# Optimization experiments

Measured on AMD Instinct MI355X. Metric: run time of the kernel, lower is better.

## Reference

```python
import jax, jax.numpy as jnp
import numpy as np

B = 1024
D = 768          # 2 * hidden_size
HID = 384        # hidden_size (split point for mu/sigma)
MLP_H = 300      # InfoNCE hidden size
LOG2PI = float(np.log(2.0 * np.pi))


def setup_inputs() -> dict:
    key = jax.random.key(0)
    ks = jax.random.split(key, 12)
    s = 0.02
    return {
        "zl": jax.random.normal(ks[0], (B, 20, D), jnp.float32),
        "zv": jax.random.normal(ks[1], (B, 36, D), jnp.float32),
        "fc_l_w": jax.random.normal(ks[2], (20,), jnp.float32) * s,
        "fc_l_b": jax.random.normal(ks[3], (), jnp.float32) * s,
        "fc_v_w": jax.random.normal(ks[4], (36,), jnp.float32) * s,
        "fc_v_b": jax.random.normal(ks[5], (), jnp.float32) * s,
        "W1": jax.random.normal(ks[6], (MLP_H, 2 * HID), jnp.float32) * s,
        "b1": jnp.zeros((MLP_H,), jnp.float32),
        "W2": jax.random.normal(ks[7], (1, MLP_H), jnp.float32) * s,
        "b2": jnp.zeros((1,), jnp.float32),
        "eps1": jax.random.normal(ks[8], (B, HID), jnp.float32),
        "eps2": jax.random.normal(ks[9], (B, HID), jnp.float32),
        "perm": jax.random.permutation(ks[10], B),
    }


def _log_prob(mu, sigma, x):
    # Independent(Normal(mu, sigma), 1).log_prob(x)
    z = (x - mu) / sigma
    return jnp.sum(-jnp.log(sigma) - 0.5 * LOG2PI - 0.5 * z * z, axis=-1)


def reference(zl, zv, fc_l_w, fc_l_b, fc_v_w, fc_v_b, W1, b1, W2, b2, eps1, eps2, perm):
    # fc over token dim: permute(0,2,1) @ Linear(20->1) -> [B, D]
    z1 = jnp.einsum('bsd,s->bd', zl, fc_l_w) + fc_l_b
    z2 = jnp.einsum('bsd,s->bd', zv, fc_v_w) + fc_v_b

    mu1, sig1 = z1[:, :HID], jax.nn.softplus(z1[:, HID:]) + 1e-7
    mu2, sig2 = z2[:, :HID], jax.nn.softplus(z2[:, HID:]) + 1e-7

    # rsample
    s1 = mu1 + sig1 * eps1  # [B, HID]
    s2 = mu2 + sig2 * eps2

    kl_1_2 = _log_prob(mu1, sig1, s1) - _log_prob(mu2, sig2, s1)
    kl_2_1 = _log_prob(mu2, sig2, s2) - _log_prob(mu1, sig1, s2)
    d_skl = jnp.mean(kl_1_2 + kl_2_1) / 2.0

    # InfoNCE(x=s1, y=s2): F(x,y) = softplus(relu([x,y]W1^T + b1) W2^T + b2)
    W1x, W1y = W1[:, :HID], W1[:, HID:]
    Ax = s1 @ W1x.T            # [B, MLP_H], x contribution
    By = s2 @ W1y.T            # [B, MLP_H], y contribution
    w2 = W2[0]                 # [MLP_H]

    # T0: matched pairs
    T0 = jax.nn.softplus(jax.nn.relu(Ax + By + b1) @ w2 + b2[0])  # [B]

    # T1[i, j] = F(x_j, y_perm[i]); tile via broadcasting instead of repeat+cat
    By_p = By[perm]                                             # [B, MLP_H]
    h = jax.nn.relu(Ax[None, :, :] + By_p[:, None, :] + b1)     # [B, B, MLP_H]
    T1 = jax.nn.softplus(h @ w2 + b2[0])                        # [B, B]

    lower_bound = T0.mean() - (jax.scipy.special.logsumexp(T1, axis=1).mean() - jnp.log(jnp.float32(B)))
    return d_skl - lower_bound
```

## Files before the change

kernel.cpp:

```cpp
#include <hip/hip_runtime.h>
#include <math.h>

#define BB   1024
#define DD   768
#define HIDV 384
#define MLPH 300
#define MLPP 320

typedef float v2f __attribute__((ext_vector_type(2)));

__device__ __forceinline__ float softplusf(float x) {
    return (x > 20.f) ? x : log1pf(expf(x));
}

__device__ __forceinline__ void f4arr(float4 v, float* o) {
    o[0] = v.x; o[1] = v.y; o[2] = v.z; o[3] = v.w;
}

__global__ void k_init(float* __restrict__ ws) {
    int i = blockIdx.x * 256 + threadIdx.x;
    if (i < 16 + BB) ws[i] = 0.f;
}

__global__ __launch_bounds__(384, 6) void k_rs(
    const float* __restrict__ zl, const float* __restrict__ zv,
    const float* __restrict__ wl, const float* __restrict__ blp,
    const float* __restrict__ wv, const float* __restrict__ bvp,
    const float* __restrict__ eps1, const float* __restrict__ eps2,
    float* __restrict__ s1, float* __restrict__ s2, float* __restrict__ accum)
{
    int b = blockIdx.x;
    int t = threadIdx.x;
    int half = (t >= 192) ? 1 : 0;
    int col = t - half * 192;
    int ofl = half * 10;
    int ofv = half * 18;
    const float4* zl4 = (const float4*)zl + b * (20 * 192) + ofl * 192 + col;
    const float4* zv4 = (const float4*)zv + b * (36 * 192) + ofv * 192 + col;

    float z1v[4] = {0,0,0,0}, z2v[4] = {0,0,0,0};

    #pragma unroll
    for (int sp = 0; sp < 10; ++sp) {
        float w = wl[sp + ofl];
        float a[4];
        f4arr(zl4[sp * 192], a);
        #pragma unroll
        for (int j = 0; j < 4; ++j) z1v[j] = fmaf(a[j], w, z1v[j]);
    }
    #pragma unroll
    for (int sp = 0; sp < 18; ++sp) {
        float w = wv[sp + ofv];
        float a[4];
        f4arr(zv4[sp * 192], a);
        #pragma unroll
        for (int j = 0; j < 4; ++j) z2v[j] = fmaf(a[j], w, z2v[j]);
    }

    __shared__ __align__(16) float p1[192 * 4];
    __shared__ __align__(16) float p2[192 * 4];
    if (half) {
        ((float4*)p1)[col] = make_float4(z1v[0], z1v[1], z1v[2], z1v[3]);
        ((float4*)p2)[col] = make_float4(z2v[0], z2v[1], z2v[2], z2v[3]);
    }
    __syncthreads();
    if (!half) {
        float q1[4], q2[4];
        f4arr(((const float4*)p1)[col], q1);
        f4arr(((const float4*)p2)[col], q2);
        #pragma unroll
        for (int j = 0; j < 4; ++j) { z1v[j] += q1[j]; z2v[j] += q2[j]; }
    }

    float bl = blp[0], bv = bvp[0];

    __shared__ __align__(16) float sg1s[HIDV];
    __shared__ __align__(16) float sg2s[HIDV];

    if (!half && col >= 96) {
        float o1[4], o2[4];
        #pragma unroll
        for (int j = 0; j < 4; ++j) {
            o1[j] = softplusf(z1v[j] + bl) + 1e-7f;
            o2[j] = softplusf(z2v[j] + bv) + 1e-7f;
        }
        ((float4*)sg1s)[col - 96] = make_float4(o1[0], o1[1], o1[2], o1[3]);
        ((float4*)sg2s)[col - 96] = make_float4(o2[0], o2[1], o2[2], o2[3]);
    }
    __syncthreads();

    float con = 0.f;
    if (!half && col < 96) {
        float e1v[4], e2v[4], g1[4], g2[4];
        f4arr(((const float4*)eps1)[b * 96 + col], e1v);
        f4arr(((const float4*)eps2)[b * 96 + col], e2v);
        f4arr(((const float4*)sg1s)[col], g1);
        f4arr(((const float4*)sg2s)[col], g2);
        float s1o[4], s2o[4];
        #pragma unroll
        for (int j = 0; j < 4; ++j) {
            float mu1 = z1v[j] + bl;
            float mu2 = z2v[j] + bv;
            float sg1 = g1[j], sg2 = g2[j];
            float e1 = e1v[j], e2 = e2v[j];
            float sv1 = fmaf(sg1, e1, mu1);
            float sv2 = fmaf(sg2, e2, mu2);
            s1o[j] = sv1; s2o[j] = sv2;
            float z12 = (sv1 - mu2) / sg2;
            float z21 = (sv2 - mu1) / sg1;
            con += -0.5f * (e1 * e1 + e2 * e2) + 0.5f * z12 * z12 + 0.5f * z21 * z21;
        }
        ((float4*)s1)[b * 96 + col] = make_float4(s1o[0], s1o[1], s1o[2], s1o[3]);
        ((float4*)s2)[b * 96 + col] = make_float4(s2o[0], s2o[1], s2o[2], s2o[3]);
    }

    #pragma unroll
    for (int m = 1; m < 64; m <<= 1) con += __shfl_xor(con, m);
    __shared__ float pr[6];
    if ((t & 63) == 0) pr[t >> 6] = con;
    __syncthreads();
    if (t == 0) {
        float s = pr[0] + pr[1] + pr[2] + pr[3] + pr[4] + pr[5];
        atomicAdd(&accum[0], s);
    }
}

__global__ __launch_bounds__(256) void k_gemm(
    const float* __restrict__ s1, const float* __restrict__ s2,
    const float* __restrict__ W1, const float* __restrict__ b1,
    float* __restrict__ Axb, float* __restrict__ By)
{
    __shared__ __align__(16) float Ss[32][36];
    __shared__ __align__(16) float Ws[32][68];
    int z = blockIdx.z;
    const float* S = z ? s2 : s1;
    float* Out = z ? By : Axb;
    int wofs = z ? HIDV : 0;
    int b0 = blockIdx.x * 32;
    int k0 = blockIdx.y * 64;
    int tid = threadIdx.x;
    int srow = tid >> 3, sc = tid & 7;
    int wrow = tid >> 2, wc = tid & 3;
    int krow = k0 + wrow;
    int tx = tid & 15, ty = tid >> 4;

    float4 ps, pw[2];
    auto ld = [&](int hc) {
        ps = *(const float4*)&S[(b0 + srow) * HIDV + hc + sc * 4];
        #pragma unroll
        for (int u = 0; u < 2; ++u)
            pw[u] = (krow < MLPH) ? *(const float4*)&W1[krow * DD + wofs + hc + wc * 4 + u * 16]
                                  : make_float4(0.f, 0.f, 0.f, 0.f);
    };
    ld(0);
    v2f acc[2][2];
    acc[0][0] = (v2f){0.f, 0.f}; acc[0][1] = (v2f){0.f, 0.f};
    acc[1][0] = (v2f){0.f, 0.f}; acc[1][1] = (v2f){0.f, 0.f};

    for (int ch = 0; ch < 12; ++ch) {
        __syncthreads();
        Ss[sc * 4 + 0][srow] = ps.x; Ss[sc * 4 + 1][srow] = ps.y;
        Ss[sc * 4 + 2][srow] = ps.z; Ss[sc * 4 + 3][srow] = ps.w;
        #pragma unroll
        for (int u = 0; u < 2; ++u) {
            int hb = wc * 4 + u * 16;
            Ws[hb + 0][wrow] = pw[u].x; Ws[hb + 1][wrow] = pw[u].y;
            Ws[hb + 2][wrow] = pw[u].z; Ws[hb + 3][wrow] = pw[u].w;
        }
        __syncthreads();
        if (ch < 11) ld((ch + 1) * 32);
        #pragma unroll
        for (int h = 0; h < 32; ++h) {
            v2f sv = *(const v2f*)&Ss[h][ty * 2];
            float4 wq = *(const float4*)&Ws[h][tx * 4];
            v2f w0 = (v2f){wq.x, wq.y};
            v2f w1 = (v2f){wq.z, wq.w};
            v2f s0 = (v2f){sv.x, sv.x};
            v2f s1b = (v2f){sv.y, sv.y};
            acc[0][0] = __builtin_elementwise_fma(s0, w0, acc[0][0]);
            acc[0][1] = __builtin_elementwise_fma(s0, w1, acc[0][1]);
            acc[1][0] = __builtin_elementwise_fma(s1b, w0, acc[1][0]);
            acc[1][1] = __builtin_elementwise_fma(s1b, w1, acc[1][1]);
        }
    }
    #pragma unroll
    for (int i = 0; i < 2; ++i) {
        int bb = b0 + ty * 2 + i;
        float vraw[4] = {acc[i][0].x, acc[i][0].y, acc[i][1].x, acc[i][1].y};
        float o[4];
        #pragma unroll
        for (int j = 0; j < 4; ++j) {
            int k = k0 + tx * 4 + j;
            float v = vraw[j];
            if (!z) v += b1[k < MLPH ? k : 0];
            o[j] = (k < MLPH) ? v : 0.f;
        }
        *(float4*)&Out[bb * MLPP + k0 + tx * 4] = make_float4(o[0], o[1], o[2], o[3]);
    }
}

__global__ void k_t0(const float* __restrict__ Axb, const float* __restrict__ By,
                     const float* __restrict__ W2, const float* __restrict__ b2,
                     float* __restrict__ accum)
{
    int b = blockIdx.x;
    int l = threadIdx.x;
    float t = 0.f;
    for (int k = l; k < MLPH; k += 64)
        t = fmaf(fmaxf(Axb[b * MLPP + k] + By[b * MLPP + k], 0.f), W2[k], t);
    #pragma unroll
    for (int m = 1; m < 64; m <<= 1) t += __shfl_xor(t, m);
    if (l == 0) atomicAdd(&accum[1], softplusf(t + b2[0]));
}

__global__ __launch_bounds__(256) void k_pairs(
    const float* __restrict__ Axb, const float* __restrict__ By,
    const int* __restrict__ perm, const float* __restrict__ W2,
    const float* __restrict__ b2, float* __restrict__ sumexp)
{
    __shared__ __align__(16) float As[64][68];
    __shared__ __align__(16) float Bs[64][68];
    __shared__ float w2s[MLPP];
    int tid = threadIdx.x;
    int j0 = blockIdx.x * 64;
    int i0 = blockIdx.y * 64;
    for (int t = tid; t < MLPP; t += 256) w2s[t] = (t < MLPH) ? W2[t] : 0.f;
    int r = tid >> 2;
    int c4 = tid & 3;
    int tx = tid & 15, ty = tid >> 4;
    int prow = perm[i0 + r];

    float4 pa[4], pb[4];
    auto ld = [&](int kc) {
        #pragma unroll
        for (int u = 0; u < 4; ++u) {
            int kq = (c4 + 4 * u) * 4;
            pa[u] = *(const float4*)&Axb[(j0 + r) * MLPP + kc + kq];
            pb[u] = *(const float4*)&By[prow * MLPP + kc + kq];
        }
    };
    ld(0);
    v2f acc2[4][2];
    #pragma unroll
    for (int c = 0; c < 4; ++c) {
        acc2[c][0] = (v2f){0.f, 0.f};
        acc2[c][1] = (v2f){0.f, 0.f};
    }
    for (int ch = 0; ch < 5; ++ch) {
        __syncthreads();
        #pragma unroll
        for (int u = 0; u < 4; ++u) {
            int kq = (c4 + 4 * u) * 4;
            As[kq + 0][r] = pa[u].x; As[kq + 1][r] = pa[u].y;
            As[kq + 2][r] = pa[u].z; As[kq + 3][r] = pa[u].w;
            Bs[kq + 0][r] = pb[u].x; Bs[kq + 1][r] = pb[u].y;
            Bs[kq + 2][r] = pb[u].z; Bs[kq + 3][r] = pb[u].w;
        }
        __syncthreads();
        if (ch < 4) ld((ch + 1) * 64);
        int kc = ch * 64;
        #pragma unroll
        for (int k = 0; k < 64; ++k) {
            float w = w2s[kc + k];
            v2f wv2 = (v2f){w, w};
            float4 af = *(const float4*)&As[k][tx * 4];
            float4 bf = *(const float4*)&Bs[k][ty * 4];
            v2f a2[2] = { (v2f){af.x, af.y}, (v2f){af.z, af.w} };
            float bs[4] = {bf.x, bf.y, bf.z, bf.w};
            #pragma unroll
            for (int c = 0; c < 4; ++c) {
                v2f bc = (v2f){bs[c], bs[c]};
                #pragma unroll
                for (int d2 = 0; d2 < 2; ++d2) {
                    v2f tv = a2[d2] + bc;
                    tv = __builtin_elementwise_max(tv, (v2f){0.f, 0.f});
                    acc2[c][d2] = __builtin_elementwise_fma(tv, wv2, acc2[c][d2]);
                }
            }
        }
    }
    float b2v = b2[0];
    #pragma unroll
    for (int c = 0; c < 4; ++c) {
        float vv[4] = {acc2[c][0].x, acc2[c][0].y, acc2[c][1].x, acc2[c][1].y};
        float ssum = 0.f;
        #pragma unroll
        for (int d = 0; d < 4; ++d)
            ssum += 1.f + expf(vv[d] + b2v);
        ssum += __shfl_xor(ssum, 1);
        ssum += __shfl_xor(ssum, 2);
        ssum += __shfl_xor(ssum, 4);
        ssum += __shfl_xor(ssum, 8);
        if (tx == 0) atomicAdd(&sumexp[i0 + ty * 4 + c], ssum);
    }
}

__global__ __launch_bounds__(256) void k_final(
    const float* __restrict__ accum, const float* __restrict__ sumexp,
    float* __restrict__ out)
{
    int tid = threadIdx.x;
    float s = 0.f;
    for (int i = tid; i < BB; i += 256) s += logf(sumexp[i]);
    #pragma unroll
    for (int m = 1; m < 64; m <<= 1) s += __shfl_xor(s, m);
    __shared__ float red[4];
    if ((tid & 63) == 0) red[tid >> 6] = s;
    __syncthreads();
    if (tid == 0) {
        float lse_mean = (red[0] + red[1] + red[2] + red[3]) / (float)BB;
        float d_skl = accum[0] / (2.f * (float)BB);
        float t0_mean = accum[1] / (float)BB;
        float lower = t0_mean - (lse_mean - logf((float)BB));
        out[0] = d_skl - lower;
    }
}

extern "C" void kernel_launch(void* const* d_in, const int* in_sizes, int n_in,
                              void* d_out, int out_size, void* d_ws, size_t ws_size,
                              hipStream_t stream)
{
    const float* zl     = (const float*)d_in[0];
    const float* zv     = (const float*)d_in[1];
    const float* fc_l_w = (const float*)d_in[2];
    const float* fc_l_b = (const float*)d_in[3];
    const float* fc_v_w = (const float*)d_in[4];
    const float* fc_v_b = (const float*)d_in[5];
    const float* W1     = (const float*)d_in[6];
    const float* b1     = (const float*)d_in[7];
    const float* W2     = (const float*)d_in[8];
    const float* b2     = (const float*)d_in[9];
    const float* eps1   = (const float*)d_in[10];
    const float* eps2   = (const float*)d_in[11];
    const int*   perm   = (const int*)d_in[12];
    float* out = (float*)d_out;

    float* ws     = (float*)d_ws;
    float* accum  = ws;
    float* sumexp = ws + 16;
    float* s1     = ws + 16 + BB;
    float* s2     = s1 + BB * HIDV;
    float* Axb    = s2 + BB * HIDV;
    float* By     = Axb + BB * MLPP;

    k_init<<<5, 256, 0, stream>>>(ws);
    k_rs<<<BB, 384, 0, stream>>>(zl, zv, fc_l_w, fc_l_b, fc_v_w, fc_v_b,
                                 eps1, eps2, s1, s2, accum);
    k_gemm<<<dim3(32, 5, 2), 256, 0, stream>>>(s1, s2, W1, b1, Axb, By);
    k_t0<<<BB, 64, 0, stream>>>(Axb, By, W2, b2, accum);
    k_pairs<<<dim3(16, 16), 256, 0, stream>>>(Axb, By, perm, W2, b2, sumexp);
    k_final<<<1, 256, 0, stream>>>(accum, sumexp, out);
}
```

Measured before the change: 312.6 us.

## Stream token-reduction inputs via async global-to-LDS copies with staged pipelining

Rewrites the token-dimension reduction kernel to use 256 threads with four waves, each handling a slice of the token rows. Rows are copied directly from global memory into LDS with global_load_lds in double-buffered stages, with manual vmcnt/lgkmcnt waits so loads overlap with the FMAs. Per-wave partial sums are then combined through LDS. The aim is to raise memory-level parallelism on the dominant ~150MB read, at the cost of about 60KB of LDS per block, which lowers occupancy, and fragile hand-written waitcnt ordering.

```diff
diff --git a/kernel.cpp b/kernel.cpp
--- a/kernel.cpp
+++ b/kernel.cpp
@@ -9,6 +9,9 @@
 
 typedef float v2f __attribute__((ext_vector_type(2)));
 
+typedef const __attribute__((address_space(1))) void* gas_t;
+typedef __attribute__((address_space(3))) void* las_t;
+
 __device__ __forceinline__ float softplusf(float x) {
     return (x > 20.f) ? x : log1pf(expf(x));
 }
@@ -16,86 +19,194 @@
 __device__ __forceinline__ void f4arr(float4 v, float* o) {
     o[0] = v.x; o[1] = v.y; o[2] = v.z; o[3] = v.w;
 }
+
+__device__ __forceinline__ void cp16(const float* g, float* l) {
+    __builtin_amdgcn_global_load_lds((gas_t)g, (las_t)l, 16, 0, 0);
+}
+
+#define WAITVM(n)  asm volatile("s_waitcnt vmcnt(" #n ")" ::: "memory")
+#define WAITLGKM() asm volatile("s_waitcnt lgkmcnt(0)" ::: "memory")
 
 __global__ void k_init(float* __restrict__ ws) {
     int i = blockIdx.x * 256 + threadIdx.x;
     if (i < 16 + BB) ws[i] = 0.f;
 }
 
-__global__ __launch_bounds__(384, 6) void k_rs(
+__global__ __launch_bounds__(256) void k_rs(
     const float* __restrict__ zl, const float* __restrict__ zv,
     const float* __restrict__ wl, const float* __restrict__ blp,
     const float* __restrict__ wv, const float* __restrict__ bvp,
     const float* __restrict__ eps1, const float* __restrict__ eps2,
     float* __restrict__ s1, float* __restrict__ s2, float* __restrict__ accum)
 {
-    int b = blockIdx.x;
-    int t = threadIdx.x;
-    int half = (t >= 192) ? 1 : 0;
-    int col = t - half * 192;
-    int ofl = half * 10;
-    int ofv = half * 18;
-    const float4* zl4 = (const float4*)zl + b * (20 * 192) + ofl * 192 + col;
-    const float4* zv4 = (const float4*)zv + b * (36 * 192) + ofv * 192 + col;
-
+    __shared__ float LA[9216];
+    __shared__ float LB[6144];
+    int tid = threadIdx.x, w = tid >> 6, l = tid & 63, b = blockIdx.x;
+
+    const float* zlb = zl + b * 15360;
+    const float* zvb = zv + b * 27648;
+    const float* gA0 = zlb + (w * 5 + 0) * 768 + l * 4;
+    const float* gB0 = zlb + (w * 5 + 3) * 768 + l * 4;
+    const float* gA1 = zvb + (w * 9 + 0) * 768 + l * 4;
+    const float* gB1 = zvb + (w * 9 + 3) * 768 + l * 4;
+    const float* gA2 = zvb + (w * 9 + 5) * 768 + l * 4;
+    const float* gB2 = zvb + (w * 9 + 8) * 768 + l * 4;
+    float* sA = LA + w * 2304;
+    float* sB = LB + w * 1536;
+
+    float wl_r[5], wv_r[9];
+    #pragma unroll
+    for (int r = 0; r < 5; ++r) wl_r[r] = wl[w * 5 + r];
+    #pragma unroll
+    for (int r = 0; r < 9; ++r) wv_r[r] = wv[w * 9 + r];
+    WAITVM(0);
+
+    float a1[3][4] = {{0.f}}, a2[3][4] = {{0.f}};
+
+    #pragma unroll
+    for (int r = 0; r < 3; ++r)
+        #pragma unroll
+        for (int c = 0; c < 3; ++c)
+            cp16(gA0 + r * 768 + c * 256, sA + r * 768 + c * 256);
+    #pragma unroll
+    for (int r = 0; r < 2; ++r)
+        #pragma unroll
+        for (int c = 0; c < 3; ++c)
+            cp16(gB0 + r * 768 + c * 256, sB + r * 768 + c * 256);
+
+    WAITVM(6);
+    #pragma unroll
+    for (int r = 0; r < 3; ++r) {
+        float ws_ = wl_r[r];
+        #pragma unroll
+        for (int c = 0; c < 3; ++c) {
+            float v[4]; f4arr(*(const float4*)(sA + r * 768 + c * 256 + l * 4), v);
+            #pragma unroll
+            for (int j = 0; j < 4; ++j) a1[c][j] = fmaf(v[j], ws_, a1[c][j]);
+        }
+    }
+    WAITLGKM();
+    #pragma unroll
+    for (int r = 0; r < 3; ++r)
+        #pragma unroll
+        for (int c = 0; c < 3; ++c)
+            cp16(gA1 + r * 768 + c * 256, sA + r * 768 + c * 256);
+
+    WAITVM(9);
+    #pragma unroll
+    for (int r = 0; r < 2; ++r) {
+        float ws_ = wl_r[3 + r];
+        #pragma unroll
+        for (int c = 0; c < 3; ++c) {
+            float v[4]; f4arr(*(const float4*)(sB + r * 768 + c * 256 + l * 4), v);
+            #pragma unroll
+            for (int j = 0; j < 4; ++j) a1[c][j] = fmaf(v[j], ws_, a1[c][j]);
+        }
+    }
+    WAITLGKM();
+    #pragma unroll
+    for (int r = 0; r < 2; ++r)
+        #pragma unroll
+        for (int c = 0; c < 3; ++c)
+            cp16(gB1 + r * 768 + c * 256, sB + r * 768 + c * 256);
+
+    WAITVM(6);
+    #pragma unroll
+    for (int r = 0; r < 3; ++r) {
+        float ws_ = wv_r[r];
+        #pragma unroll
+        for (int c = 0; c < 3; ++c) {
+            float v[4]; f4arr(*(const float4*)(sA + r * 768 + c * 256 + l * 4), v);
+            #pragma unroll
+            for (int j = 0; j < 4; ++j) a2[c][j] = fmaf(v[j], ws_, a2[c][j]);
+        }
+    }
+    WAITLGKM();
+    #pragma unroll
+    for (int r = 0; r < 3; ++r)
+        #pragma unroll
+        for (int c = 0; c < 3; ++c)
+            cp16(gA2 + r * 768 + c * 256, sA + r * 768 + c * 256);
+
+    WAITVM(9);
+    #pragma unroll
+    for (int r = 0; r < 2; ++r) {
+        float ws_ = wv_r[3 + r];
+        #pragma unroll
+        for (int c = 0; c < 3; ++c) {
+            float v[4]; f4arr(*(const float4*)(sB + r * 768 + c * 256 + l * 4), v);
+            #pragma unroll
+            for (int j = 0; j < 4; ++j) a2[c][j] = fmaf(v[j], ws_, a2[c][j]);
+        }
+    }
+    WAITLGKM();
+    #pragma unroll
+    for (int c = 0; c < 3; ++c)
+        cp16(gB2 + c * 256, sB + c * 256);
+
+    WAITVM(3);
+    #pragma unroll
+    for (int r = 0; r < 3; ++r) {
+        float ws_ = wv_r[5 + r];
+        #pragma unroll
+        for (int c = 0; c < 3; ++c) {
+            float v[4]; f4arr(*(const float4*)(sA + r * 768 + c * 256 + l * 4), v);
+            #pragma unroll
+            for (int j = 0; j < 4; ++j) a2[c][j] = fmaf(v[j], ws_, a2[c][j]);
+        }
+    }
+    WAITVM(0);
+    {
+        float ws_ = wv_r[8];
+        #pragma unroll
+        for (int c = 0; c < 3; ++c) {
+            float v[4]; f4arr(*(const float4*)(sB + c * 256 + l * 4), v);
+            #pragma unroll
+            for (int j = 0; j < 4; ++j) a2[c][j] = fmaf(v[j], ws_, a2[c][j]);
+        }
+    }
+
+    #pragma unroll
+    for (int c = 0; c < 3; ++c) {
+        *(float4*)(LA + w * 2304 + (c * 64 + l) * 4) =
+            make_float4(a1[c][0], a1[c][1], a1[c][2], a1[c][3]);
+        *(float4*)(LA + w * 2304 + 768 + (c * 64 + l) * 4) =
+            make_float4(a2[c][0], a2[c][1], a2[c][2], a2[c][3]);
+    }
+    __syncthreads();
+
+    float bl = blp[0], bv = bvp[0];
     float z1v[4] = {0,0,0,0}, z2v[4] = {0,0,0,0};
-
-    #pragma unroll
-    for (int sp = 0; sp < 10; ++sp) {
-        float w = wl[sp + ofl];
-        float a[4];
-        f4arr(zl4[sp * 192], a);
-        #pragma unroll
-        for (int j = 0; j < 4; ++j) z1v[j] = fmaf(a[j], w, z1v[j]);
-    }
-    #pragma unroll
-    for (int sp = 0; sp < 18; ++sp) {
-        float w = wv[sp + ofv];
-        float a[4];
-        f4arr(zv4[sp * 192], a);
-        #pragma unroll
-        for (int j = 0; j < 4; ++j) z2v[j] = fmaf(a[j], w, z2v[j]);
-    }
-
-    __shared__ __align__(16) float p1[192 * 4];
-    __shared__ __align__(16) float p2[192 * 4];
-    if (half) {
-        ((float4*)p1)[col] = make_float4(z1v[0], z1v[1], z1v[2], z1v[3]);
-        ((float4*)p2)[col] = make_float4(z2v[0], z2v[1], z2v[2], z2v[3]);
+    if (tid < 192) {
+        #pragma unroll
+        for (int w2 = 0; w2 < 4; ++w2) {
+            float q1[4], q2[4];
+            f4arr(*(const float4*)(LA + w2 * 2304 + tid * 4), q1);
+            f4arr(*(const float4*)(LA + w2 * 2304 + 768 + tid * 4), q2);
+            #pragma unroll
+            for (int j = 0; j < 4; ++j) { z1v[j] += q1[j]; z2v[j] += q2[j]; }
+        }
     }
     __syncthreads();
-    if (!half) {
-        float q1[4], q2[4];
-        f4arr(((const float4*)p1)[col], q1);
-        f4arr(((const float4*)p2)[col], q2);
-        #pragma unroll
-        for (int j = 0; j < 4; ++j) { z1v[j] += q1[j]; z2v[j] += q2[j]; }
-    }
-
-    float bl = blp[0], bv = bvp[0];
-
-    __shared__ __align__(16) float sg1s[HIDV];
-    __shared__ __align__(16) float sg2s[HIDV];
-
-    if (!half && col >= 96) {
+    if (tid >= 96 && tid < 192) {
         float o1[4], o2[4];
         #pragma unroll
         for (int j = 0; j < 4; ++j) {
             o1[j] = softplusf(z1v[j] + bl) + 1e-7f;
             o2[j] = softplusf(z2v[j] + bv) + 1e-7f;
         }
-        ((float4*)sg1s)[col - 96] = make_float4(o1[0], o1[1], o1[2], o1[3]);
-        ((float4*)sg2s)[col - 96] = make_float4(o2[0], o2[1], o2[2], o2[3]);
+        *(float4*)(LB + (tid - 96) * 4)       = make_float4(o1[0], o1[1], o1[2], o1[3]);
+        *(float4*)(LB + 384 + (tid - 96) * 4) = make_float4(o2[0], o2[1], o2[2], o2[3]);
     }
     __syncthreads();
 
     float con = 0.f;
-    if (!half && col < 96) {
+    if (tid < 96) {
         float e1v[4], e2v[4], g1[4], g2[4];
-        f4arr(((const float4*)eps1)[b * 96 + col], e1v);
-        f4arr(((const float4*)eps2)[b * 96 + col], e2v);
-        f4arr(((const float4*)sg1s)[col], g1);
-        f4arr(((const float4*)sg2s)[col], g2);
+        f4arr(((const float4*)eps1)[b * 96 + tid], e1v);
+        f4arr(((const float4*)eps2)[b * 96 + tid], e2v);
+        f4arr(*(const float4*)(LB + tid * 4), g1);
+        f4arr(*(const float4*)(LB + 384 + tid * 4), g2);
         float s1o[4], s2o[4];
         #pragma unroll
         for (int j = 0; j < 4; ++j) {
@@ -110,19 +221,16 @@
             float z21 = (sv2 - mu1) / sg1;
             con += -0.5f * (e1 * e1 + e2 * e2) + 0.5f * z12 * z12 + 0.5f * z21 * z21;
         }
-        ((float4*)s1)[b * 96 + col] = make_float4(s1o[0], s1o[1], s1o[2], s1o[3]);
-        ((float4*)s2)[b * 96 + col] = make_float4(s2o[0], s2o[1], s2o[2], s2o[3]);
+        ((float4*)s1)[b * 96 + tid] = make_float4(s1o[0], s1o[1], s1o[2], s1o[3]);
+        ((float4*)s2)[b * 96 + tid] = make_float4(s2o[0], s2o[1], s2o[2], s2o[3]);
     }
 
     #pragma unroll
     for (int m = 1; m < 64; m <<= 1) con += __shfl_xor(con, m);
-    __shared__ float pr[6];
-    if ((t & 63) == 0) pr[t >> 6] = con;
+    __shared__ float pr[4];
+    if ((tid & 63) == 0) pr[tid >> 6] = con;
     __syncthreads();
-    if (t == 0) {
-        float s = pr[0] + pr[1] + pr[2] + pr[3] + pr[4] + pr[5];
-        atomicAdd(&accum[0], s);
-    }
+    if (tid == 0) atomicAdd(&accum[0], pr[0] + pr[1] + pr[2] + pr[3]);
 }
 
 __global__ __launch_bounds__(256) void k_gemm(
@@ -344,7 +452,7 @@
     float* By     = Axb + BB * MLPP;
 
     k_init<<<5, 256, 0, stream>>>(ws);
-    k_rs<<<BB, 384, 0, stream>>>(zl, zv, fc_l_w, fc_l_b, fc_v_w, fc_v_b,
+    k_rs<<<BB, 256, 0, stream>>>(zl, zv, fc_l_w, fc_l_b, fc_v_w, fc_v_b,
                                  eps1, eps2, s1, s2, accum);
     k_gemm<<<dim3(32, 5, 2), 256, 0, stream>>>(s1, s2, W1, b1, Axb, By);
     k_t0<<<BB, 64, 0, stream>>>(Axb, By, W2, b2, accum);
```

Result: no change. 310.6 us (-0.7%).
